# Kernel tuning notes

Hardware: AMD Instinct MI355X
Metric: run time of the kernel (lower is better)

The kernel has to match this reference:

```python
import jax, jax.numpy as jnp
import numpy as np

DIM = 256
HEADS = 8
HEAD_DIM = DIM // HEADS          # 32 (v head dim, also defines scale)
QK_DIM = DIM // HEADS // 2       # 16 (q/k head dim)
SCALE = HEAD_DIM ** -0.5


def conv3x3(x, w, b):
    # x: [B,C,H,W], w: [O,I,3,3] (torch OIHW), padding=1 stride=1 == SAME
    y = jax.lax.conv_general_dilated(
        x, w, window_strides=(1, 1), padding='SAME',
        dimension_numbers=('NCHW', 'OIHW', 'NCHW'))
    return y + b[None, :, None, None]


def setup_inputs() -> dict:
    key = jax.random.key(0)
    ks = jax.random.split(key, 12)
    s = 0.02
    B, C, H, W = 1, DIM, 64, 64
    return {
        'x':       jax.random.normal(ks[0], (B, C, H, W), jnp.float32),
        'attn_kv': jax.random.normal(ks[1], (B, C, H, W), jnp.float32),
        'qw':  jax.random.normal(ks[2], (C, C, 3, 3), jnp.float32) * s,
        'qb':  jnp.zeros((C,), jnp.float32),
        'kvw': jax.random.normal(ks[3], (C, C, 3, 3), jnp.float32) * s,
        'kvb': jnp.zeros((C,), jnp.float32),
        'Wq':  jax.random.normal(ks[4], (C // 2, C), jnp.float32) * s,
        'bq':  jnp.zeros((C // 2,), jnp.float32),
        'Wk':  jax.random.normal(ks[5], (C // 2, C), jnp.float32) * s,
        'bk':  jnp.zeros((C // 2,), jnp.float32),
        'Wv':  jax.random.normal(ks[6], (C, C), jnp.float32) * s,
        'bv':  jnp.zeros((C,), jnp.float32),
        'Wp':  jax.random.normal(ks[7], (C, C), jnp.float32) * s,
        'bp':  jnp.zeros((C,), jnp.float32),
    }


def reference(x, attn_kv, qw, qb, kvw, kvb, Wq, bq, Wk, bk, Wv, bv, Wp, bp):
    B, C, Hh, Ww = x.shape
    N = Hh * Ww
    # conv projections
    xq = conv3x3(x, qw, qb)            # [B,C,H,W]
    kv = conv3x3(attn_kv, kvw, kvb)    # [B,C,H,W]
    # flatten to tokens [B,N,C]
    xf = xq.reshape(B, C, N).transpose(0, 2, 1)
    kvf = kv.reshape(B, C, N).transpose(0, 2, 1)
    # qkv projections with asymmetric head dims
    q = (xf @ Wq.T + bq).reshape(B, N, HEADS, QK_DIM).transpose(0, 2, 1, 3)    # [B,h,N,16]
    k = (kvf @ Wk.T + bk).reshape(B, N, HEADS, QK_DIM).transpose(0, 2, 1, 3)   # [B,h,N,16]
    v = (kvf @ Wv.T + bv).reshape(B, N, HEADS, HEAD_DIM).transpose(0, 2, 1, 3) # [B,h,N,32]
    # attention (manual softmax(q k^T) v)
    attn = jax.nn.softmax(jnp.einsum('bhnd,bhmd->bhnm', q * SCALE, k), axis=-1)  # [B,h,N,N]
    o = jnp.einsum('bhnm,bhmd->bhnd', attn, v)  # [B,h,N,32]
    # replicate the original transpose(1,2).reshape(B,N,C) on the [1,B,h,N,dv]
    # tensor: memory order becomes (h, B, N, dv) flattened into (B, N, C).
    o = jnp.transpose(o, (1, 0, 2, 3)).reshape(B, N, C)
    out = o @ Wp.T + bp                               # [B,N,C]
    return out.transpose(0, 2, 1).reshape(B, C, Hh, Ww)
```

## Files before the change

kernel.cpp:

```cpp
#include <hip/hip_runtime.h>

typedef unsigned short u16;
typedef __attribute__((ext_vector_type(8))) short bf16x8;
typedef __attribute__((ext_vector_type(4))) float f32x4;
typedef __attribute__((ext_vector_type(16))) float f32x16;
typedef __attribute__((ext_vector_type(4))) unsigned u32x4;
typedef __attribute__((ext_vector_type(2))) int i32x2;

struct alignas(8) u16x4 { u16 x, y, z, w; };

#define MFMA16(A, B, C) __builtin_amdgcn_mfma_f32_16x16x32_bf16(A, B, C, 0, 0, 0)
#define MFMA32(A, B, C) __builtin_amdgcn_mfma_f32_32x32x16_bf16(A, B, C, 0, 0, 0)
#define QSCALE (0.17677669529663689f * 1.4426950408889634f)

__device__ __forceinline__ u16 f2bf(float f) {
  unsigned u = __float_as_uint(f);
  u = (u + 0x7fffu + ((u >> 16) & 1u)) >> 16;
  return (u16)u;
}

__device__ __forceinline__ bf16x8 ldb8(const u16* p) {
  return *reinterpret_cast<const bf16x8*>(p);
}

__device__ __forceinline__ void glds16(const u16* g, u16* l) {
  __builtin_amdgcn_global_load_lds(
      (const __attribute__((address_space(1))) void*)g,
      (__attribute__((address_space(3))) void*)l, 16, 0, 0);
}

__global__ __launch_bounds__(256) void prep_kernel(
    const float* __restrict__ x, const float* __restrict__ akv,
    const float* __restrict__ qw, const float* __restrict__ kvw,
    const float* __restrict__ Wq, const float* __restrict__ Wk,
    const float* __restrict__ Wv, const float* __restrict__ Wp,
    u16* __restrict__ xpT, u16* __restrict__ w2,
    u16* __restrict__ wqs, u16* __restrict__ wks,
    u16* __restrict__ wvs, u16* __restrict__ wps)
{
  __shared__ float sm[64 * 65];
  const int b = blockIdx.x, t = threadIdx.x;
  if (b < 512) {
    const int z = b >> 8, rem = b & 255;
    const int cib = (rem >> 6) * 64, y = rem & 63;
    const float* in = (z ? akv : x);
    const int tc = t & 63, tr = t >> 6;
    #pragma unroll
    for (int i = 0; i < 16; ++i) {
      const int ci = i * 4 + tr;
      sm[ci * 65 + tc] = in[(size_t)(cib + ci) * 4096 + y * 64 + tc];
    }
    __syncthreads();
    u16* dst = xpT + (size_t)z * 4356 * 256;
    #pragma unroll
    for (int i = 0; i < 16; ++i) {
      const int px = i * 4 + tr;
      dst[(size_t)((y + 1) * 66 + px + 1) * 256 + cib + tc] = f2bf(sm[tc * 65 + px]);
    }
    return;
  }
  if (b < 642) {
    const int slot = (b - 512) * 4 + (t >> 6);
    const int z = slot >= 260 ? 1 : 0;
    const int j = slot - z * 260;
    int pos;
    if (j < 66) pos = j;
    else if (j < 132) pos = 65 * 66 + (j - 66);
    else { const int j2 = j - 132; pos = (1 + (j2 >> 1)) * 66 + (j2 & 1) * 65; }
    u16x4 zr = {0, 0, 0, 0};
    *reinterpret_cast<u16x4*>(xpT + (size_t)z * 4356 * 256 + (size_t)pos * 256 + (t & 63) * 4) = zr;
    return;
  }
  if (b < 1154) {
    const int idx = b - 642;
    const int z = idx >> 8, co = idx & 255;
    const float* src = (z ? kvw : qw) + (size_t)co * 2304;
    u16* dst = w2 + (size_t)z * 256 * 2304 + (size_t)co * 2304;
    #pragma unroll
    for (int i = 0; i < 9; ++i) sm[i * 256 + t] = src[i * 256 + t];
    __syncthreads();
    #pragma unroll
    for (int i = 0; i < 9; ++i) dst[i * 256 + t] = f2bf(sm[t * 9 + i]);
    return;
  }
  {
    int idx = (b - 1154) * 256 + t;
    if (idx < 32768) { wqs[idx] = f2bf(Wq[idx] * QSCALE); return; }
    idx -= 32768;
    if (idx < 32768) { wks[idx] = f2bf(Wk[idx]); return; }
    idx -= 32768;
    if (idx < 65536) { wvs[idx] = f2bf(Wv[idx]); return; }
    idx -= 65536;
    wps[idx] = f2bf(Wp[idx]);
  }
}

__global__ __launch_bounds__(256, 2) void conv_kernel(
    const u16* __restrict__ xpT, const u16* __restrict__ w2,
    const float* __restrict__ qb, const float* __restrict__ kvb,
    u16* __restrict__ xqt, u16* __restrict__ kvt)
{
  __shared__ u16 ab[3][64 * 64];
  __shared__ u16 bb[3][64 * 64];

  const int z = blockIdx.z;
  const u16* __restrict__ X = xpT + (size_t)z * 4356 * 256;
  const u16* __restrict__ W = w2 + (size_t)z * 256 * 2304;
  const float* bias = z ? kvb : qb;
  u16* out = z ? kvt : xqt;

  const int lane = threadIdx.x & 63, w = threadIdx.x >> 6;
  const int lo = lane & 15, g = lane >> 4;
  const int r8 = lane >> 3, c = lane & 7;
  const int wr = w >> 1, wc = w & 1;
  const int cobase = blockIdx.x * 64;
  const int tbase = blockIdx.y * 64;

  const bool isA = (w < 2);
  const u16* gb[4];
  int ldso[4];
  #pragma unroll
  for (int q = 0; q < 4; ++q) {
    const int flat = w * 4 + q;
    if (flat < 8) {
      const int j = flat;
      gb[q] = W + (size_t)(cobase + j * 8 + r8) * 2304 + (c ^ r8) * 8;
      ldso[q] = j * 512;
    } else {
      const int j = flat - 8;
      const int tok = tbase + j * 8 + r8;
      const int padrow = ((tok >> 6) + 1) * 66 + (tok & 63) + 1;
      gb[q] = X + (size_t)padrow * 256 + (c ^ r8) * 8;
      ldso[q] = j * 512;
    }
  }

  f32x4 acc[2][2] = {};

  auto stage = [&](int s, int bsel) {
    int srcoff;
    if (isA) {
      srcoff = s * 64;
    } else {
      const int kk = s >> 2;
      const int koff = (kk / 3 - 1) * 66 + (kk % 3) - 1;
      srcoff = koff * 256 + (s & 3) * 64;
    }
    u16* lb = isA ? ab[bsel] : bb[bsel];
    #pragma unroll
    for (int q = 0; q < 4; ++q)
      glds16(gb[q] + srcoff, lb + ldso[q]);
  };

  stage(0, 0);
  stage(1, 1);
  asm volatile("s_waitcnt vmcnt(4)" ::: "memory");
  __syncthreads();

  #pragma unroll 1
  for (int s = 0; s < 36; ++s) {
    const int cur = s % 3;
    if (s + 2 < 36) stage(s + 2, (s + 2) % 3);
    #pragma unroll
    for (int ks = 0; ks < 2; ++ks) {
      const int swz = ((ks * 4 + g) ^ (lo & 7)) * 8;
      const int rowA = wr * 32 + lo, colB = wc * 32 + lo;
      bf16x8 a0 = *reinterpret_cast<const bf16x8*>(&ab[cur][rowA * 64 + swz]);
      bf16x8 a1 = *reinterpret_cast<const bf16x8*>(&ab[cur][(rowA + 16) * 64 + swz]);
      bf16x8 b0 = *reinterpret_cast<const bf16x8*>(&bb[cur][colB * 64 + swz]);
      bf16x8 b1 = *reinterpret_cast<const bf16x8*>(&bb[cur][(colB + 16) * 64 + swz]);
      acc[0][0] = MFMA16(a0, b0, acc[0][0]);
      acc[0][1] = MFMA16(a0, b1, acc[0][1]);
      acc[1][0] = MFMA16(a1, b0, acc[1][0]);
      acc[1][1] = MFMA16(a1, b1, acc[1][1]);
    }
    if (s < 35) {
      if (s + 2 < 36) asm volatile("s_waitcnt vmcnt(4)" ::: "memory");
      else            asm volatile("s_waitcnt vmcnt(0)" ::: "memory");
      __syncthreads();
    }
  }

  #pragma unroll
  for (int af = 0; af < 2; ++af) {
    const int cb = cobase + wr * 32 + af * 16 + 4 * g;
    const float4 bi = *reinterpret_cast<const float4*>(bias + cb);
    #pragma unroll
    for (int bf = 0; bf < 2; ++bf) {
      const int t = tbase + wc * 32 + bf * 16 + lo;
      f32x4 v = acc[af][bf];
      u16x4 pk = { f2bf(v[0] + bi.x), f2bf(v[1] + bi.y),
                   f2bf(v[2] + bi.z), f2bf(v[3] + bi.w) };
      *reinterpret_cast<u16x4*>(out + (size_t)t * 256 + cb) = pk;
    }
  }
}

__global__ __launch_bounds__(256) void qkv_kernel(
    const u16* __restrict__ xqt, const u16* __restrict__ kvt,
    const u16* __restrict__ wqs, const u16* __restrict__ wks,
    const u16* __restrict__ wvs,
    const float* __restrict__ bq, const float* __restrict__ bk,
    const float* __restrict__ bv,
    u16* __restrict__ Qh, u16* __restrict__ Kh, u16* __restrict__ Vp)
{
  const int lane = threadIdx.x & 63, wid = threadIdx.x >> 6;
  const int lo = lane & 15, g = lane >> 4;
  const int bx = blockIdx.x;

  if (blockIdx.z == 0) {
    const bool isq = bx < 2;
    const u16* A = isq ? wqs : wks;
    const u16* Bm = isq ? xqt : kvt;
    const float* bias = isq ? bq : bk;
    const float bsc = isq ? (float)QSCALE : 1.f;
    u16* outp = isq ? Qh : Kh;
    const int c0 = (bx & 1) * 64 + (wid >> 1) * 32;
    const int n0 = blockIdx.y * 64 + (wid & 1) * 32;

    const u16* Ar0 = A + (c0 + lo) * 256 + 8 * g;
    const u16* Ar1 = A + (c0 + 16 + lo) * 256 + 8 * g;
    const u16* Br0 = Bm + (n0 + lo) * 256 + 8 * g;
    const u16* Br1 = Bm + (n0 + 16 + lo) * 256 + 8 * g;

    f32x4 acc[2][2] = {};
    bf16x8 A0 = ldb8(Ar0), A1 = ldb8(Ar1), B0 = ldb8(Br0), B1 = ldb8(Br1);
    #pragma unroll
    for (int s = 0; s < 8; ++s) {
      bf16x8 A0n, A1n, B0n, B1n;
      if (s < 7) {
        const int kn = (s + 1) * 32;
        A0n = ldb8(Ar0 + kn); A1n = ldb8(Ar1 + kn);
        B0n = ldb8(Br0 + kn); B1n = ldb8(Br1 + kn);
      }
      acc[0][0] = MFMA16(A0, B0, acc[0][0]);
      acc[0][1] = MFMA16(A0, B1, acc[0][1]);
      acc[1][0] = MFMA16(A1, B0, acc[1][0]);
      acc[1][1] = MFMA16(A1, B1, acc[1][1]);
      A0 = A0n; A1 = A1n; B0 = B0n; B1 = B1n;
    }
    #pragma unroll
    for (int af = 0; af < 2; ++af) {
      const int cb = c0 + af * 16 + 4 * g;
      const int h = cb >> 4, dd = cb & 15;
      const float4 bi = *reinterpret_cast<const float4*>(bias + cb);
      #pragma unroll
      for (int bfr = 0; bfr < 2; ++bfr) {
        const int n = n0 + bfr * 16 + lo;
        f32x4 v = acc[af][bfr];
        u16x4 pk = { f2bf(v[0] + bi.x * bsc), f2bf(v[1] + bi.y * bsc),
                     f2bf(v[2] + bi.z * bsc), f2bf(v[3] + bi.w * bsc) };
        *reinterpret_cast<u16x4*>(outp + h * 65536 + n * 16 + dd) = pk;
      }
    }
  } else {
    const int n0 = blockIdx.y * 64 + (wid >> 1) * 32;
    const int c0 = bx * 64 + (wid & 1) * 32;

    const u16* Ar0 = kvt + (n0 + lo) * 256 + 8 * g;
    const u16* Ar1 = kvt + (n0 + 16 + lo) * 256 + 8 * g;
    const u16* Br0 = wvs + (c0 + lo) * 256 + 8 * g;
    const u16* Br1 = wvs + (c0 + 16 + lo) * 256 + 8 * g;

    f32x4 acc[2][2] = {};
    bf16x8 A0 = ldb8(Ar0), A1 = ldb8(Ar1), B0 = ldb8(Br0), B1 = ldb8(Br1);
    #pragma unroll
    for (int s = 0; s < 8; ++s) {
      bf16x8 A0n, A1n, B0n, B1n;
      if (s < 7) {
        const int kn = (s + 1) * 32;
        A0n = ldb8(Ar0 + kn); A1n = ldb8(Ar1 + kn);
        B0n = ldb8(Br0 + kn); B1n = ldb8(Br1 + kn);
      }
      acc[0][0] = MFMA16(A0, B0, acc[0][0]);
      acc[0][1] = MFMA16(A0, B1, acc[0][1]);
      acc[1][0] = MFMA16(A1, B0, acc[1][0]);
      acc[1][1] = MFMA16(A1, B1, acc[1][1]);
      A0 = A0n; A1 = A1n; B0 = B0n; B1 = B1n;
    }
    #pragma unroll
    for (int af = 0; af < 2; ++af) {
      const int nb = n0 + af * 16 + 4 * g;
      const int tblk = nb >> 4, hhalf = (nb >> 3) & 1, j0 = nb & 7;
      #pragma unroll
      for (int bfr = 0; bfr < 2; ++bfr) {
        const int cc = c0 + bfr * 16 + lo;
        const int h = cc >> 5, dv = cc & 31;
        const float bi = bv[cc];
        f32x4 v = acc[af][bfr];
        u16x4 pk = { f2bf(v[0] + bi), f2bf(v[1] + bi),
                     f2bf(v[2] + bi), f2bf(v[3] + bi) };
        *reinterpret_cast<u16x4*>(
            Vp + (size_t)h * 131072 + tblk * 512 + hhalf * 256 + dv * 8 + j0) = pk;
      }
    }
  }
}

__global__ __launch_bounds__(512, 4) void attn_kernel(
    const u16* __restrict__ Qh, const u16* __restrict__ Kh,
    const u16* __restrict__ Vp, u16* __restrict__ O2)
{
  __shared__ float olds[16][8][64];
  __shared__ float l_ldsA[8][32], l_ldsB[8][32];
  __shared__ float invA[32], invB[32];

  const int lane = threadIdx.x & 63, w = threadIdx.x >> 6;
  const int lo = lane & 31, hi = lane >> 5;
  const int bx = blockIdx.x;
  const int h = bx & 7, qg = bx >> 3;
  const int qt0 = qg * 64;

  const u16* Q = Qh + h * 65536;
  const u16* K = Kh + h * 65536;

  const bf16x8 qbA = ldb8(Q + (qt0 + lo) * 16 + 8 * hi);
  const bf16x8 qbB = ldb8(Q + (qt0 + 32 + lo) * 16 + 8 * hi);

  f32x16 oA = {0,0,0,0,0,0,0,0,0,0,0,0,0,0,0,0};
  f32x16 oB = {0,0,0,0,0,0,0,0,0,0,0,0,0,0,0,0};
  float lA0 = 0.f, lA1 = 0.f, lB0 = 0.f, lB1 = 0.f;
  const int kvbase = w * 512;

  const u16* kptr = K + (kvbase + lo) * 16 + 8 * hi;
  const u16* vptr = Vp + (size_t)h * 131072 + (size_t)kvbase * 32 + lane * 8;

  bf16x8 kb = ldb8(kptr);
  bf16x8 vb0 = ldb8(vptr);
  bf16x8 vb1 = ldb8(vptr + 512);

  #pragma unroll 1
  for (int st = 0; st < 16; ++st) {
    kptr += 512; vptr += 1024;
    const bf16x8 kb_n = ldb8(kptr);
    const bf16x8 vb0_n = ldb8(vptr);
    const bf16x8 vb1_n = ldb8(vptr + 512);

    const f32x16 zf = {0,0,0,0,0,0,0,0,0,0,0,0,0,0,0,0};
    f32x16 sA = MFMA32(kb, qbA, zf);
    f32x16 sB = MFMA32(kb, qbB, zf);

    {
      unsigned cpk[8];
      #pragma unroll
      for (int r = 0; r < 16; r += 2) {
        const float p0 = __builtin_amdgcn_exp2f(sA[r]);
        const float p1 = __builtin_amdgcn_exp2f(sA[r + 1]);
        lA0 += p0; lA1 += p1;
        asm("v_cvt_pk_bf16_f32 %0, %1, %2" : "=v"(cpk[r >> 1]) : "v"(p0), "v"(p1));
      }
      u32x4 fa0, fa1;
      { i32x2 r2 = __builtin_amdgcn_permlane32_swap((int)cpk[0], (int)cpk[2], false, false);
        fa0[0] = (unsigned)r2[0]; fa0[2] = (unsigned)r2[1]; }
      { i32x2 r2 = __builtin_amdgcn_permlane32_swap((int)cpk[1], (int)cpk[3], false, false);
        fa0[1] = (unsigned)r2[0]; fa0[3] = (unsigned)r2[1]; }
      { i32x2 r2 = __builtin_amdgcn_permlane32_swap((int)cpk[4], (int)cpk[6], false, false);
        fa1[0] = (unsigned)r2[0]; fa1[2] = (unsigned)r2[1]; }
      { i32x2 r2 = __builtin_amdgcn_permlane32_swap((int)cpk[5], (int)cpk[7], false, false);
        fa1[1] = (unsigned)r2[0]; fa1[3] = (unsigned)r2[1]; }
      oA = MFMA32(__builtin_bit_cast(bf16x8, fa0), vb0, oA);
      oA = MFMA32(__builtin_bit_cast(bf16x8, fa1), vb1, oA);
    }
    {
      unsigned cpk[8];
      #pragma unroll
      for (int r = 0; r < 16; r += 2) {
        const float p0 = __builtin_amdgcn_exp2f(sB[r]);
        const float p1 = __builtin_amdgcn_exp2f(sB[r + 1]);
        lB0 += p0; lB1 += p1;
        asm("v_cvt_pk_bf16_f32 %0, %1, %2" : "=v"(cpk[r >> 1]) : "v"(p0), "v"(p1));
      }
      u32x4 fa0, fa1;
      { i32x2 r2 = __builtin_amdgcn_permlane32_swap((int)cpk[0], (int)cpk[2], false, false);
        fa0[0] = (unsigned)r2[0]; fa0[2] = (unsigned)r2[1]; }
      { i32x2 r2 = __builtin_amdgcn_permlane32_swap((int)cpk[1], (int)cpk[3], false, false);
        fa0[1] = (unsigned)r2[0]; fa0[3] = (unsigned)r2[1]; }
      { i32x2 r2 = __builtin_amdgcn_permlane32_swap((int)cpk[4], (int)cpk[6], false, false);
        fa1[0] = (unsigned)r2[0]; fa1[2] = (unsigned)r2[1]; }
      { i32x2 r2 = __builtin_amdgcn_permlane32_swap((int)cpk[5], (int)cpk[7], false, false);
        fa1[1] = (unsigned)r2[0]; fa1[3] = (unsigned)r2[1]; }
      oB = MFMA32(__builtin_bit_cast(bf16x8, fa0), vb0, oB);
      oB = MFMA32(__builtin_bit_cast(bf16x8, fa1), vb1, oB);
    }
    kb = kb_n; vb0 = vb0_n; vb1 = vb1_n;
  }

  float lA = lA0 + lA1;  lA += __shfl_xor(lA, 32);
  float lB = lB0 + lB1;  lB += __shfl_xor(lB, 32);
  if (lane < 32) { l_ldsA[w][lane] = lA; l_ldsB[w][lane] = lB; }

  #pragma unroll
  for (int r = 0; r < 16; ++r) olds[r][w][lane] = oA[r];
  __syncthreads();

  if (w == 0 && lane < 32) {
    float L = 0.f;
    #pragma unroll
    for (int w2 = 0; w2 < 8; ++w2) L += l_ldsA[w2][lane];
    invA[lane] = 1.0f / L;
  }
  if (w == 1 && lane < 32) {
    float L = 0.f;
    #pragma unroll
    for (int w2 = 0; w2 < 8; ++w2) L += l_ldsB[w2][lane];
    invB[lane] = 1.0f / L;
  }
  __syncthreads();

  #pragma unroll
  for (int j = 0; j < 2; ++j) {
    const int r = 2 * w + j;
    const int q = (r & 3) + 8 * (r >> 2) + 4 * hi;
    float acc = 0.f;
    #pragma unroll
    for (int w2 = 0; w2 < 8; ++w2) acc += olds[r][w2][lane];
    acc *= invA[q];
    const int n = qt0 + q;
    O2[(size_t)((h << 9) + (n >> 3)) * 256 + ((n & 7) << 5) + lo] = f2bf(acc);
  }
  __syncthreads();

  #pragma unroll
  for (int r = 0; r < 16; ++r) olds[r][w][lane] = oB[r];
  __syncthreads();

  #pragma unroll
  for (int j = 0; j < 2; ++j) {
    const int r = 2 * w + j;
    const int q = (r & 3) + 8 * (r >> 2) + 4 * hi;
    float acc = 0.f;
    #pragma unroll
    for (int w2 = 0; w2 < 8; ++w2) acc += olds[r][w2][lane];
    acc *= invB[q];
    const int n = qt0 + 32 + q;
    O2[(size_t)((h << 9) + (n >> 3)) * 256 + ((n & 7) << 5) + lo] = f2bf(acc);
  }
}

__global__ __launch_bounds__(256) void oproj_kernel(
    const u16* __restrict__ O2, const u16* __restrict__ wps,
    const float* __restrict__ bp, float* __restrict__ outp)
{
  const int lane = threadIdx.x & 63, wid = threadIdx.x >> 6;
  const int lo = lane & 15, g = lane >> 4;
  const int n0 = blockIdx.x * 64 + (wid >> 1) * 32;
  const int c0 = blockIdx.y * 64 + (wid & 1) * 32;

  f32x4 acc[2][2] = {};
  #pragma unroll
  for (int s = 0; s < 8; ++s) {
    const int k0 = s * 32 + 8 * g;
    bf16x8 A0 = ldb8(O2 + (n0 + lo) * 256 + k0);
    bf16x8 A1 = ldb8(O2 + (n0 + 16 + lo) * 256 + k0);
    bf16x8 B0 = ldb8(wps + (c0 + lo) * 256 + k0);
    bf16x8 B1 = ldb8(wps + (c0 + 16 + lo) * 256 + k0);
    acc[0][0] = MFMA16(A0, B0, acc[0][0]);
    acc[0][1] = MFMA16(A0, B1, acc[0][1]);
    acc[1][0] = MFMA16(A1, B0, acc[1][0]);
    acc[1][1] = MFMA16(A1, B1, acc[1][1]);
  }
  #pragma unroll
  for (int af = 0; af < 2; ++af) {
    const int nb = n0 + af * 16 + 4 * g;
    #pragma unroll
    for (int bfr = 0; bfr < 2; ++bfr) {
      const int c = c0 + bfr * 16 + lo;
      const float bi = bp[c];
      f32x4 v = acc[af][bfr];
      float4 r4;
      r4.x = v[0] + bi; r4.y = v[1] + bi; r4.z = v[2] + bi; r4.w = v[3] + bi;
      *reinterpret_cast<float4*>(outp + (size_t)c * 4096 + nb) = r4;
    }
  }
}

extern "C" void kernel_launch(void* const* d_in, const int* in_sizes, int n_in,
                              void* d_out, int out_size, void* d_ws, size_t ws_size,
                              hipStream_t stream) {
  (void)in_sizes; (void)n_in; (void)out_size; (void)ws_size;
  const float* x   = (const float*)d_in[0];
  const float* akv = (const float*)d_in[1];
  const float* qw  = (const float*)d_in[2];
  const float* qb  = (const float*)d_in[3];
  const float* kvw = (const float*)d_in[4];
  const float* kvb = (const float*)d_in[5];
  const float* Wq  = (const float*)d_in[6];
  const float* bq  = (const float*)d_in[7];
  const float* Wk  = (const float*)d_in[8];
  const float* bk  = (const float*)d_in[9];
  const float* Wv  = (const float*)d_in[10];
  const float* bv  = (const float*)d_in[11];
  const float* Wp  = (const float*)d_in[12];
  const float* bp  = (const float*)d_in[13];
  float* outp = (float*)d_out;

  char* wsb = (char*)d_ws;
  size_t off = 0;
  auto take = [&](size_t bytes) {
    char* p = wsb + off;
    off = (off + bytes + 255) & ~(size_t)255;
    return p;
  };
  u16* xpT = (u16*)take(2ULL * 4356 * 256 * 2);
  u16* w2  = (u16*)take(2ULL * 256 * 2304 * 2);
  u16* wqs = (u16*)take(128ULL * 256 * 2);
  u16* wks = (u16*)take(128ULL * 256 * 2);
  u16* wvs = (u16*)take(256ULL * 256 * 2);
  u16* wps = (u16*)take(256ULL * 256 * 2);
  u16* xqt = (u16*)take(4096ULL * 256 * 2);
  u16* kvt = (u16*)take(4096ULL * 256 * 2);
  u16* Qh  = (u16*)take(8ULL * 4096 * 16 * 2);
  u16* Kh  = (u16*)take(8ULL * 4096 * 16 * 2);
  u16* Vp  = (u16*)take(8ULL * 131072 * 2);
  u16* O2  = (u16*)take(4096ULL * 256 * 2);

  prep_kernel<<<dim3(1922), dim3(256), 0, stream>>>(
      x, akv, qw, kvw, Wq, Wk, Wv, Wp, xpT, w2, wqs, wks, wvs, wps);
  conv_kernel<<<dim3(4, 64, 2), dim3(256), 0, stream>>>(xpT, w2, qb, kvb, xqt, kvt);
  qkv_kernel<<<dim3(4, 64, 2), dim3(256), 0, stream>>>(
      xqt, kvt, wqs, wks, wvs, bq, bk, bv, Qh, Kh, Vp);
  attn_kernel<<<dim3(512), dim3(512), 0, stream>>>(Qh, Kh, Vp, O2);
  oproj_kernel<<<dim3(64, 4), dim3(256), 0, stream>>>(O2, wps, bp, outp);
}
```

Before: 70.07 us.

## Split attention KV range across two blocks and combine partials in output projection

The attention grid is doubled so each block handles half of the key/value sequence. Unnormalized fp32 partial outputs and row sums go to workspace, and the output-projection kernel merges and normalizes them before the bf16 MFMA. The goal is more parallelism on a GPU where 512 blocks may underfill the device. The cost is extra fp32 global traffic, per-element conversion work in oproj, and loss of the software prefetch of K/V in the loop.

```diff
diff --git a/kernel.cpp b/kernel.cpp
--- a/kernel.cpp
+++ b/kernel.cpp
@@ -3,6 +3,7 @@
 typedef unsigned short u16;
 typedef __attribute__((ext_vector_type(8))) short bf16x8;
 typedef __attribute__((ext_vector_type(4))) float f32x4;
+typedef __attribute__((ext_vector_type(8))) float f32x8;
 typedef __attribute__((ext_vector_type(16))) float f32x16;
 typedef __attribute__((ext_vector_type(4))) unsigned u32x4;
 typedef __attribute__((ext_vector_type(2))) int i32x2;
@@ -299,16 +300,18 @@
 
 __global__ __launch_bounds__(512, 4) void attn_kernel(
     const u16* __restrict__ Qh, const u16* __restrict__ Kh,
-    const u16* __restrict__ Vp, u16* __restrict__ O2)
+    const u16* __restrict__ Vp, float* __restrict__ Of,
+    float* __restrict__ Lf)
 {
   __shared__ float olds[16][8][64];
   __shared__ float l_ldsA[8][32], l_ldsB[8][32];
-  __shared__ float invA[32], invB[32];
 
   const int lane = threadIdx.x & 63, w = threadIdx.x >> 6;
   const int lo = lane & 31, hi = lane >> 5;
   const int bx = blockIdx.x;
-  const int h = bx & 7, qg = bx >> 3;
+  const int h = bx & 7;
+  const int qg = (bx >> 3) & 63;
+  const int half = bx >> 9;
   const int qt0 = qg * 64;
 
   const u16* Q = Qh + h * 65536;
@@ -320,21 +323,17 @@
   f32x16 oA = {0,0,0,0,0,0,0,0,0,0,0,0,0,0,0,0};
   f32x16 oB = {0,0,0,0,0,0,0,0,0,0,0,0,0,0,0,0};
   float lA0 = 0.f, lA1 = 0.f, lB0 = 0.f, lB1 = 0.f;
-  const int kvbase = w * 512;
+  const int kvbase = half * 2048 + w * 256;
 
   const u16* kptr = K + (kvbase + lo) * 16 + 8 * hi;
   const u16* vptr = Vp + (size_t)h * 131072 + (size_t)kvbase * 32 + lane * 8;
 
-  bf16x8 kb = ldb8(kptr);
-  bf16x8 vb0 = ldb8(vptr);
-  bf16x8 vb1 = ldb8(vptr + 512);
-
   #pragma unroll 1
-  for (int st = 0; st < 16; ++st) {
+  for (int st = 0; st < 8; ++st) {
+    const bf16x8 kb = ldb8(kptr);
+    const bf16x8 vb0 = ldb8(vptr);
+    const bf16x8 vb1 = ldb8(vptr + 512);
     kptr += 512; vptr += 1024;
-    const bf16x8 kb_n = ldb8(kptr);
-    const bf16x8 vb0_n = ldb8(vptr);
-    const bf16x8 vb1_n = ldb8(vptr + 512);
 
     const f32x16 zf = {0,0,0,0,0,0,0,0,0,0,0,0,0,0,0,0};
     f32x16 sA = MFMA32(kb, qbA, zf);
@@ -382,13 +381,15 @@
       oB = MFMA32(__builtin_bit_cast(bf16x8, fa0), vb0, oB);
       oB = MFMA32(__builtin_bit_cast(bf16x8, fa1), vb1, oB);
     }
-    kb = kb_n; vb0 = vb0_n; vb1 = vb1_n;
   }
 
   float lA = lA0 + lA1;  lA += __shfl_xor(lA, 32);
   float lB = lB0 + lB1;  lB += __shfl_xor(lB, 32);
   if (lane < 32) { l_ldsA[w][lane] = lA; l_ldsB[w][lane] = lB; }
 
+  float* Ofh = Of + (size_t)half * 4096 * 256;
+  float* Lfh = Lf + half * 32768 + h * 4096;
+
   #pragma unroll
   for (int r = 0; r < 16; ++r) olds[r][w][lane] = oA[r];
   __syncthreads();
@@ -397,15 +398,14 @@
     float L = 0.f;
     #pragma unroll
     for (int w2 = 0; w2 < 8; ++w2) L += l_ldsA[w2][lane];
-    invA[lane] = 1.0f / L;
+    Lfh[qt0 + lane] = L;
   }
   if (w == 1 && lane < 32) {
     float L = 0.f;
     #pragma unroll
     for (int w2 = 0; w2 < 8; ++w2) L += l_ldsB[w2][lane];
-    invB[lane] = 1.0f / L;
-  }
-  __syncthreads();
+    Lfh[qt0 + 32 + lane] = L;
+  }
 
   #pragma unroll
   for (int j = 0; j < 2; ++j) {
@@ -414,9 +414,8 @@
     float acc = 0.f;
     #pragma unroll
     for (int w2 = 0; w2 < 8; ++w2) acc += olds[r][w2][lane];
-    acc *= invA[q];
     const int n = qt0 + q;
-    O2[(size_t)((h << 9) + (n >> 3)) * 256 + ((n & 7) << 5) + lo] = f2bf(acc);
+    Ofh[(size_t)((h << 9) + (n >> 3)) * 256 + ((n & 7) << 5) + lo] = acc;
   }
   __syncthreads();
 
@@ -431,33 +430,51 @@
     float acc = 0.f;
     #pragma unroll
     for (int w2 = 0; w2 < 8; ++w2) acc += olds[r][w2][lane];
-    acc *= invB[q];
     const int n = qt0 + 32 + q;
-    O2[(size_t)((h << 9) + (n >> 3)) * 256 + ((n & 7) << 5) + lo] = f2bf(acc);
+    Ofh[(size_t)((h << 9) + (n >> 3)) * 256 + ((n & 7) << 5) + lo] = acc;
   }
 }
 
 __global__ __launch_bounds__(256) void oproj_kernel(
-    const u16* __restrict__ O2, const u16* __restrict__ wps,
-    const float* __restrict__ bp, float* __restrict__ outp)
+    const float* __restrict__ Of, const float* __restrict__ Lf,
+    const u16* __restrict__ wps, const float* __restrict__ bp,
+    float* __restrict__ outp)
 {
   const int lane = threadIdx.x & 63, wid = threadIdx.x >> 6;
   const int lo = lane & 15, g = lane >> 4;
   const int n0 = blockIdx.x * 64 + (wid >> 1) * 32;
   const int c0 = blockIdx.y * 64 + (wid & 1) * 32;
 
+  const float* O1 = Of;
+  const float* O2f = Of + (size_t)4096 * 256;
+  const float* L1 = Lf;
+  const float* L2 = Lf + 32768;
+
   f32x4 acc[2][2] = {};
   #pragma unroll
   for (int s = 0; s < 8; ++s) {
     const int k0 = s * 32 + 8 * g;
-    bf16x8 A0 = ldb8(O2 + (n0 + lo) * 256 + k0);
-    bf16x8 A1 = ldb8(O2 + (n0 + 16 + lo) * 256 + k0);
+
+    bf16x8 Afr[2];
+    #pragma unroll
+    for (int af = 0; af < 2; ++af) {
+      const int row = n0 + af * 16 + lo;
+      const size_t off = (size_t)row * 256 + k0;
+      const f32x8 a = *reinterpret_cast<const f32x8*>(O1 + off);
+      const f32x8 b = *reinterpret_cast<const f32x8*>(O2f + off);
+      const int li = (row >> 9) * 4096 + ((row & 511) << 3) + s;
+      const float inv = 1.0f / (L1[li] + L2[li]);
+      union { bf16x8 v; u16 e[8]; } rr;
+      #pragma unroll
+      for (int j = 0; j < 8; ++j) rr.e[j] = f2bf((a[j] + b[j]) * inv);
+      Afr[af] = rr.v;
+    }
     bf16x8 B0 = ldb8(wps + (c0 + lo) * 256 + k0);
     bf16x8 B1 = ldb8(wps + (c0 + 16 + lo) * 256 + k0);
-    acc[0][0] = MFMA16(A0, B0, acc[0][0]);
-    acc[0][1] = MFMA16(A0, B1, acc[0][1]);
-    acc[1][0] = MFMA16(A1, B0, acc[1][0]);
-    acc[1][1] = MFMA16(A1, B1, acc[1][1]);
+    acc[0][0] = MFMA16(Afr[0], B0, acc[0][0]);
+    acc[0][1] = MFMA16(Afr[0], B1, acc[0][1]);
+    acc[1][0] = MFMA16(Afr[1], B0, acc[1][0]);
+    acc[1][1] = MFMA16(Afr[1], B1, acc[1][1]);
   }
   #pragma unroll
   for (int af = 0; af < 2; ++af) {
@@ -512,13 +529,14 @@
   u16* Qh  = (u16*)take(8ULL * 4096 * 16 * 2);
   u16* Kh  = (u16*)take(8ULL * 4096 * 16 * 2);
   u16* Vp  = (u16*)take(8ULL * 131072 * 2);
-  u16* O2  = (u16*)take(4096ULL * 256 * 2);
+  float* Of = (float*)take(2ULL * 4096 * 256 * 4);
+  float* Lf = (float*)take(2ULL * 8 * 4096 * 4);
 
   prep_kernel<<<dim3(1922), dim3(256), 0, stream>>>(
       x, akv, qw, kvw, Wq, Wk, Wv, Wp, xpT, w2, wqs, wks, wvs, wps);
   conv_kernel<<<dim3(4, 64, 2), dim3(256), 0, stream>>>(xpT, w2, qb, kvb, xqt, kvt);
   qkv_kernel<<<dim3(4, 64, 2), dim3(256), 0, stream>>>(
       xqt, kvt, wqs, wks, wvs, bq, bk, bv, Qh, Kh, Vp);
-  attn_kernel<<<dim3(512), dim3(512), 0, stream>>>(Qh, Kh, Vp, O2);
-  oproj_kernel<<<dim3(64, 4), dim3(256), 0, stream>>>(O2, wps, bp, outp);
-}
+  attn_kernel<<<dim3(1024), dim3(512), 0, stream>>>(Qh, Kh, Vp, Of, Lf);
+  oproj_kernel<<<dim3(64, 4), dim3(256), 0, stream>>>(Of, Lf, wps, bp, outp);
+}
```

New measurement: 77.61 us. +10.8%, slower.
